# Optimization experiments

Measured on AMD Instinct MI355X. Metric: run time of the kernel, lower is better.

The kernel has to match this reference:

```python
import jax, jax.numpy as jnp
import numpy as np

N_HEAD = 16
T0 = 1.0        # eta schedule reference time
C_LOG = 3.0     # fixed eta(t) = C_LOG * log(t / T0)  (mode='log', non-learnable default)
ETA_CLIP = 50.0 # eta clamped to [-ETA_CLIP, ETA_CLIP] before exponentiation


def setup_inputs() -> dict:
    key = jax.random.key(0)
    k0, k1, k2 = jax.random.split(key, 3)
    B, T, D = 2, 2048, 1024
    x = jax.random.normal(k0, (B, T, D), dtype=jnp.float32)
    ln_weight = jnp.ones((D,), dtype=jnp.float32)  # LayerNorm weight (bias=False per cfg)
    c_attn_w = jax.random.normal(k1, (3 * D, D), dtype=jnp.float32) * 0.02  # torch Linear weight [3D, D]
    c_proj_w = jax.random.normal(k2, (D, D), dtype=jnp.float32) * 0.02      # output proj [D, D]
    # theta_h = inv_softplus(1.0) so that step size h = softplus(theta_h) = 1.0
    theta_h = jnp.asarray(np.log(np.expm1(1.0)), dtype=jnp.float32)
    return {"x": x, "ln_weight": ln_weight, "c_attn_w": c_attn_w,
            "c_proj_w": c_proj_w, "theta_h": theta_h}


def _layer_norm(x, w, eps=1e-5):
    mu = jnp.mean(x, axis=-1, keepdims=True)
    var = jnp.var(x, axis=-1, keepdims=True)
    return (x - mu) * jax.lax.rsqrt(var + eps) * w


def reference(x, ln_weight, c_attn_w, c_proj_w, theta_h):
    B, T, D = x.shape
    H = N_HEAD
    hd = D // H

    y = _layer_norm(x, ln_weight)
    qkv = jnp.einsum('btd,ed->bte', y, c_attn_w)        # [B, T, 3D]
    q, k, v = jnp.split(qkv, 3, axis=-1)
    q = q.reshape(B, T, H, hd).transpose(0, 2, 1, 3)    # [B, H, T, hd]
    k = k.reshape(B, T, H, hd).transpose(0, 2, 1, 3)
    v = v.reshape(B, T, H, hd).transpose(0, 2, 1, 3)

    # time-dependent conformal/symplectic scaling: t_i = t0 + h*i, eta = c_log*log(t/t0)
    h = jax.nn.softplus(theta_h)
    t = T0 + h * jnp.arange(T, dtype=jnp.float32)
    eta = jnp.clip(C_LOG * jnp.log(t / T0), -ETA_CLIP, ETA_CLIP)  # [T]
    q = q * jnp.exp(eta)[None, None, :, None]    # query scaled by exp(+eta(t_i))
    k = k * jnp.exp(-eta)[None, None, :, None]   # key scaled by exp(-eta(t_j))

    att = jnp.einsum('bhqd,bhkd->bhqk', q, k) / jnp.sqrt(jnp.float32(hd))
    mask = jnp.tril(jnp.ones((T, T), dtype=bool))  # causal: keep j <= i
    att = jnp.where(mask[None, None], att, -jnp.inf)
    att = jax.nn.softmax(att, axis=-1)

    out = jnp.einsum('bhqk,bhkd->bhqd', att, v)
    out = out.transpose(0, 2, 1, 3).reshape(B, T, D)
    return jnp.einsum('btd,ed->bte', out, c_proj_w)
```

## Files before the change

kernel.cpp:

```cpp
#include <hip/hip_runtime.h>
#include <stdint.h>
#include <stddef.h>

typedef __attribute__((ext_vector_type(8))) short short8;
typedef __attribute__((ext_vector_type(4))) float float4v;

#define T_SEQ 2048
#define D_MODEL 1024
#define NH 16
#define HD 64

static __device__ __forceinline__ unsigned short f2bf(float f) {
  unsigned u = __builtin_bit_cast(unsigned, f);
  u += 0x7fffu + ((u >> 16) & 1u);
  return (unsigned short)(u >> 16);
}
static __device__ __forceinline__ float bf2f(unsigned short h) {
  unsigned u = ((unsigned)h) << 16;
  return __builtin_bit_cast(float, u);
}
static __device__ __forceinline__ float4v mfma16(short8 a, short8 b, float4v c) {
  return __builtin_amdgcn_mfma_f32_16x16x32_bf16(a, b, c, 0, 0, 0);
}
static __device__ __forceinline__ void split3(float f, unsigned short& h0,
                                              unsigned short& h1, unsigned short& h2) {
  h0 = f2bf(f);
  float r1 = f - bf2f(h0);
  h1 = f2bf(r1);
  float r2 = r1 - bf2f(h1);
  h2 = f2bf(r2);
}
static __device__ __forceinline__ void split2(float f, unsigned short& h0, unsigned short& h1) {
  h0 = f2bf(f);
  h1 = f2bf(f - bf2f(h0));
}

static __device__ __forceinline__ void stage16(const unsigned short* g, unsigned short* l) {
#if __has_builtin(__builtin_amdgcn_global_load_lds)
  __builtin_amdgcn_global_load_lds(
      (const __attribute__((address_space(1))) unsigned int*)g,
      (__attribute__((address_space(3))) unsigned int*)l, 16, 0, 0);
#else
  *(short8*)l = *(const short8*)g;
#endif
}

__global__ __launch_bounds__(256) void prep_kernel(
    const float* x, const float* wgt, const float* attn_w, const float* theta,
    unsigned short* y0, unsigned short* y1, unsigned short* y2,
    unsigned short* W0, unsigned short* W1, unsigned short* W2,
    float* E, float* Einv) {
  __shared__ float rs[4], rq[4];
  int bx = blockIdx.x;
  int tid = threadIdx.x;
  if (bx < 4096) {
    int row = bx;
    const float* xr = x + (size_t)row * D_MODEL;
    float v[4];
    float sum = 0.f, ssq = 0.f;
    for (int it = 0; it < 4; ++it) {
      float f = xr[tid + 256 * it];
      v[it] = f;
      sum += f; ssq += f * f;
    }
    for (int off = 32; off >= 1; off >>= 1) {
      sum += __shfl_xor(sum, off, 64);
      ssq += __shfl_xor(ssq, off, 64);
    }
    int w = tid >> 6;
    if ((tid & 63) == 0) { rs[w] = sum; rq[w] = ssq; }
    __syncthreads();
    sum = rs[0] + rs[1] + rs[2] + rs[3];
    ssq = rq[0] + rq[1] + rq[2] + rq[3];
    float mu = sum * (1.0f / D_MODEL);
    float var = ssq * (1.0f / D_MODEL) - mu * mu;
    float rstd = rsqrtf(var + 1e-5f);
    for (int it = 0; it < 4; ++it) {
      int d = tid + 256 * it;
      float y = (v[it] - mu) * rstd * wgt[d];
      unsigned short h0, h1, h2;
      split3(y, h0, h1, h2);
      size_t o = (size_t)row * D_MODEL + d;
      y0[o] = h0; y1[o] = h1; y2[o] = h2;
    }
  } else if (bx < 5632) {
    size_t base = ((size_t)(bx - 4096) * 256 + tid) * 8;
    int row = (int)(base >> 10);
    short8 a, b, c;
    for (int j = 0; j < 8; ++j) {
      unsigned short h0, h1, h2;
      split3(attn_w[base + j], h0, h1, h2);
      a[j] = (short)h0; b[j] = (short)h1; c[j] = (short)h2;
    }
    *(short8*)(W0 + base) = a;
    *(short8*)(W1 + base) = b;
    if (row < 2048) *(short8*)(W2 + base) = c;
  } else {
    int i = (bx - 5632) * 256 + tid;
    if (i < T_SEQ) {
      float th = theta[0];
      float h = log1pf(expf(th));
      float t = 1.0f + h * (float)i;
      float eta = 3.0f * logf(t);
      eta = fminf(fmaxf(eta, -50.0f), 50.0f);
      E[i] = expf(eta);
      Einv[i] = expf(-eta);
    }
  }
}

__global__ __launch_bounds__(256) void conv_pw(const float* src, unsigned short* P0,
                                               unsigned short* P1) {
  size_t base = ((size_t)blockIdx.x * 256 + threadIdx.x) * 8;
  short8 a, b;
  for (int j = 0; j < 8; ++j) {
    unsigned short h0, h1;
    split2(src[base + j], h0, h1);
    a[j] = (short)h0; b[j] = (short)h1;
  }
  *(short8*)(P0 + base) = a;
  *(short8*)(P1 + base) = b;
}

__global__ __launch_bounds__(256) void qkv_gemm(
    const unsigned short* y0, const unsigned short* y1, const unsigned short* y2,
    const unsigned short* W0, const unsigned short* W1, const unsigned short* W2,
    const float* E, const float* Einv,
    float* Qf, unsigned short* K0, unsigned short* K1, unsigned short* K2,
    unsigned short* VbT) {
  __shared__ unsigned short SB[6 * 4096];
  int tid = threadIdx.x;
  int w = tid >> 6, lane = tid & 63, q4 = lane >> 4, ln = lane & 15;
  int wr = w >> 1, wc = w & 1;
  int m0 = blockIdx.y * 128;
  int bi = m0 >> 11;
  int m0g = m0 & 2047;
  int srow = tid >> 2, kpart = tid & 3;
  unsigned lds_off = (unsigned)tid * 16;
  float4v zero = {0.f, 0.f, 0.f, 0.f};
  float4v acc[4][4];
  for (int mt = 0; mt < 4; ++mt)
    for (int ct = 0; ct < 4; ++ct) acc[mt][ct] = zero;

  if (blockIdx.x < 16) {
    int n0g = blockIdx.x * 128;
    const unsigned short* Asrc[3] = {y0, y1, y2};
    const unsigned short* Bsrc[3] = {W0, W1, W2};
    for (int k0 = 0; k0 < D_MODEL; k0 += 32) {
      __syncthreads();
      for (int i = 0; i < 2; ++i) {
        size_t arow = (size_t)(m0 + srow + i * 64) * D_MODEL + k0 + kpart * 8;
        size_t brow = (size_t)(n0g + srow + i * 64) * D_MODEL + k0 + kpart * 8;
        for (int s = 0; s < 3; ++s) {
          stage16(Asrc[s] + arow, (unsigned short*)((char*)(SB + s * 4096) + lds_off + i * 4096));
          stage16(Bsrc[s] + brow, (unsigned short*)((char*)(SB + (3 + s) * 4096) + lds_off + i * 4096));
        }
      }
      __syncthreads();
      short8 af[4][3];
      for (int mt = 0; mt < 4; ++mt)
        for (int s = 0; s < 3; ++s)
          af[mt][s] = *(const short8*)(SB + s * 4096 + (wr * 64 + mt * 16 + ln) * 32 + q4 * 8);
      for (int ct = 0; ct < 4; ++ct) {
        int brow = (wc * 64 + ct * 16 + ln) * 32 + q4 * 8;
        short8 b0 = *(const short8*)(SB + 3 * 4096 + brow);
        short8 b1 = *(const short8*)(SB + 4 * 4096 + brow);
        short8 b2 = *(const short8*)(SB + 5 * 4096 + brow);
        for (int mt = 0; mt < 4; ++mt) {
          float4v a = acc[mt][ct];
          a = mfma16(af[mt][0], b0, a);
          a = mfma16(af[mt][1], b0, a);
          a = mfma16(af[mt][0], b1, a);
          a = mfma16(af[mt][1], b1, a);
          a = mfma16(af[mt][0], b2, a);
          a = mfma16(af[mt][2], b0, a);
          acc[mt][ct] = a;
        }
      }
    }
    int region = n0g >> 10;
    __syncthreads();
    if (region == 0) {
      float* Ql = (float*)SB;
      for (int h = 0; h < 2; ++h) {
        if (wc == h) {
          for (int mt = 0; mt < 4; ++mt)
            for (int ct = 0; ct < 4; ++ct)
              for (int r = 0; r < 4; ++r) {
                int t_loc = wr * 64 + mt * 16 + q4 * 4 + r;
                int d = ct * 16 + ln;
                int t = m0g + t_loc;
                Ql[t_loc * 64 + d] = acc[mt][ct][r] * (E[t] * 0.1803368801f);
              }
        }
        __syncthreads();
        int h_glob = ((n0g + h * 64) & 1023) >> 6;
        float* dst = Qf + ((size_t)(bi * NH + h_glob) * T_SEQ + m0g) * HD;
        for (int it = 0; it < 8; ++it) {
          int idx = it * 256 + tid;
          *(float4v*)(dst + idx * 4) = *(const float4v*)(Ql + idx * 4);
        }
        __syncthreads();
      }
    } else {
      unsigned short* Kl = SB;
      for (int h = 0; h < 2; ++h) {
        if (wc == h) {
          for (int mt = 0; mt < 4; ++mt)
            for (int ct = 0; ct < 4; ++ct)
              for (int r = 0; r < 4; ++r) {
                int t_loc = wr * 64 + mt * 16 + q4 * 4 + r;
                int d = ct * 16 + ln;
                int t = m0g + t_loc;
                unsigned short h0, h1, h2;
                split3(acc[mt][ct][r] * Einv[t], h0, h1, h2);
                Kl[t_loc * 64 + d] = h0;
                Kl[8192 + t_loc * 64 + d] = h1;
                Kl[16384 + t_loc * 64 + d] = h2;
              }
        }
        __syncthreads();
        int h_glob = ((n0g + h * 64) & 1023) >> 6;
        size_t base = ((size_t)(bi * NH + h_glob) * T_SEQ + m0g) * HD;
        unsigned short* dsts[3] = {K0 + base, K1 + base, K2 + base};
        for (int s = 0; s < 3; ++s)
          for (int it = 0; it < 4; ++it) {
            int idx = it * 256 + tid;
            *(short8*)(dsts[s] + idx * 8) = *(const short8*)(Kl + s * 8192 + idx * 8);
          }
        __syncthreads();
      }
    }
  } else {
    int n0g = (blockIdx.x - 16) * 128;
    const unsigned short* Asrc[2] = {y0, y1};
    const unsigned short* Bsrc[2] = {W0, W1};
    for (int k0 = 0; k0 < D_MODEL; k0 += 32) {
      __syncthreads();
      for (int i = 0; i < 2; ++i) {
        size_t arow = (size_t)(m0 + srow + i * 64) * D_MODEL + k0 + kpart * 8;
        size_t brow = (size_t)(2048 + n0g + srow + i * 64) * D_MODEL + k0 + kpart * 8;
        for (int s = 0; s < 2; ++s) {
          stage16(Asrc[s] + arow, (unsigned short*)((char*)(SB + s * 4096) + lds_off + i * 4096));
          stage16(Bsrc[s] + brow, (unsigned short*)((char*)(SB + (2 + s) * 4096) + lds_off + i * 4096));
        }
      }
      __syncthreads();
      short8 af[4][2];
      for (int mt = 0; mt < 4; ++mt)
        for (int s = 0; s < 2; ++s)
          af[mt][s] = *(const short8*)(SB + s * 4096 + (wr * 64 + mt * 16 + ln) * 32 + q4 * 8);
      for (int ct = 0; ct < 4; ++ct) {
        int brow = (wc * 64 + ct * 16 + ln) * 32 + q4 * 8;
        short8 b0 = *(const short8*)(SB + 2 * 4096 + brow);
        short8 b1 = *(const short8*)(SB + 3 * 4096 + brow);
        for (int mt = 0; mt < 4; ++mt) {
          float4v a = acc[mt][ct];
          a = mfma16(af[mt][0], b0, a);
          a = mfma16(af[mt][1], b0, a);
          a = mfma16(af[mt][0], b1, a);
          acc[mt][ct] = a;
        }
      }
    }
    __syncthreads();
    unsigned short* Vl = SB;
    for (int h = 0; h < 2; ++h) {
      if (wc == h) {
        for (int mt = 0; mt < 4; ++mt)
          for (int ct = 0; ct < 4; ++ct)
            for (int r = 0; r < 4; ++r) {
              int t_loc = wr * 64 + mt * 16 + q4 * 4 + r;
              int d = ct * 16 + ln;
              Vl[d * 128 + t_loc] = f2bf(acc[mt][ct][r]);
            }
      }
      __syncthreads();
      int h_glob = (n0g + h * 64) >> 6;
      size_t base = (size_t)(bi * NH + h_glob) * HD * T_SEQ + m0g;
      for (int it = 0; it < 4; ++it) {
        int idx = it * 256 + tid;
        int d = idx >> 4, c = idx & 15;
        *(short8*)(VbT + base + (size_t)d * T_SEQ + c * 8) =
            *(const short8*)(Vl + d * 128 + c * 8);
      }
      __syncthreads();
    }
  }
}

#define ATTN_STAGE(BUF, J0)                                                   \
  for (int i_ = 0; i_ < 2; ++i_) {                                            \
    size_t go_ = (size_t)((J0) + srow + i_ * 32) * 64 + scd * 8;              \
    int lo_ = tid * 8 + i_ * 2048;                                            \
    stage16(Kb0 + go_, &Ks[BUF][0][lo_]);                                     \
    stage16(Kb1 + go_, &Ks[BUF][1][lo_]);                                     \
    stage16(Kb2 + go_, &Ks[BUF][2][lo_]);                                     \
    stage16(Vb + (size_t)(srow + i_ * 32) * T_SEQ + (J0) + scd * 8,           \
            &Vs[BUF][lo_]);                                                   \
  }

#define ATTN_STEP(JT, DIAG)                                                   \
  {                                                                           \
    const int cur_ = (JT) & 1;                                                \
    float p[4][4];                                                            \
    for (int c = 0; c < 4; ++c) {                                             \
      float4v s = zero;                                                       \
      for (int ks = 0; ks < 2; ++ks) {                                        \
        int koff = ((c * 16 + ln) * 8 + ((ks * 4 + q4) ^ swz)) * 8;           \
        short8 k0v = *(const short8*)&Ks[cur_][0][koff];                      \
        short8 k1v = *(const short8*)&Ks[cur_][1][koff];                      \
        short8 k2v = *(const short8*)&Ks[cur_][2][koff];                      \
        s = mfma16(qa[ks][0], k0v, s);                                        \
        s = mfma16(qa[ks][1], k0v, s);                                        \
        s = mfma16(qa[ks][0], k1v, s);                                        \
        s = mfma16(qa[ks][1], k1v, s);                                        \
        s = mfma16(qa[ks][0], k2v, s);                                        \
        s = mfma16(qa[ks][2], k0v, s);                                        \
      }                                                                       \
      if (DIAG) {                                                             \
        int jrow = (JT) * 64 + c * 16 + ln;                                   \
        for (int r = 0; r < 4; ++r)                                           \
          if (jrow > ibase + q4 * 4 + r) s[r] = -3e38f;                       \
      }                                                                       \
      for (int r = 0; r < 4; ++r) p[c][r] = s[r];                             \
    }                                                                         \
    float alpha[4], mnew[4];                                                  \
    for (int r = 0; r < 4; ++r) {                                             \
      float tm = fmaxf(fmaxf(p[0][r], p[1][r]), fmaxf(p[2][r], p[3][r]));     \
      for (int off = 8; off >= 1; off >>= 1)                                  \
        tm = fmaxf(tm, __shfl_xor(tm, off, 16));                              \
      mnew[r] = fmaxf(m_r[r], tm);                                            \
      alpha[r] = exp2f(m_r[r] - mnew[r]);                                     \
      m_r[r] = mnew[r];                                                       \
    }                                                                         \
    for (int c = 0; c < 4; ++c)                                               \
      for (int r = 0; r < 4; ++r) p[c][r] = exp2f(p[c][r] - mnew[r]);         \
    for (int c = 0; c < 4; ++c)                                               \
      for (int r = 0; r < 4; ++r) oacc[c][r] *= alpha[r];                     \
    for (int r = 0; r < 4; ++r) lacc[r] *= alpha[r];                          \
    __asm__ __volatile__("" ::: "memory");                                    \
    for (int c = 0; c < 4; ++c)                                               \
      for (int r = 0; r < 4; ++r)                                             \
        Plds[w][q4 * 4 + r][c * 16 + ln] =                                    \
            (unsigned short)(__builtin_bit_cast(unsigned, p[c][r]) >> 16);    \
    __asm__ __volatile__("" ::: "memory");                                    \
    for (int ks = 0; ks < 2; ++ks) {                                          \
      short8 pa = *(const short8*)&Plds[w][ln][ks * 32 + q4 * 8];             \
      for (int c = 0; c < 4; ++c) {                                           \
        int voff = ((c * 16 + ln) * 8 + ((ks * 4 + q4) ^ swz)) * 8;           \
        short8 vb = *(const short8*)&Vs[cur_][voff];                          \
        oacc[c] = mfma16(pa, vb, oacc[c]);                                    \
      }                                                                       \
      lacc = mfma16(pa, ones, lacc);                                          \
    }                                                                         \
    __asm__ __volatile__("" ::: "memory");                                    \
  }

__global__ __launch_bounds__(256) void attn_kernel(
    const float* Qf, const unsigned short* K0, const unsigned short* K1,
    const unsigned short* K2, const unsigned short* VbT,
    unsigned short* Ob0, unsigned short* Ob1) {
  __shared__ unsigned short Ks[2][3][4096];
  __shared__ unsigned short Vs[2][4096];
  __shared__ unsigned short Plds[4][16][72];
  int tid = threadIdx.x;
  int w = tid >> 6, lane = tid & 63, q4 = lane >> 4, ln = lane & 15;
  int bidx = blockIdx.x;
  int bh = ((bidx & 7) << 2) | ((bidx >> 3) & 3);
  int px = bidx >> 5;
  const float* Qb = Qf + (size_t)bh * T_SEQ * HD;
  const unsigned short* Kb0 = K0 + (size_t)bh * T_SEQ * HD;
  const unsigned short* Kb1 = K1 + (size_t)bh * T_SEQ * HD;
  const unsigned short* Kb2 = K2 + (size_t)bh * T_SEQ * HD;
  const unsigned short* Vb = VbT + (size_t)bh * HD * T_SEQ;
  int b = bh >> 4, hh = bh & 15;
  float4v zero = {0.f, 0.f, 0.f, 0.f};
  short8 ones;
  for (int j = 0; j < 8; ++j) ones[j] = (short)(unsigned short)0x3F80;

  int srow = tid >> 3, scs = tid & 7;
  int scd = scs ^ (srow & 7);
  int swz = ln & 7;

  for (int half = 0; half < 2; ++half) {
    int qt = half ? (31 - px) : px;
    int q0 = qt * 64;
    int ibase = q0 + w * 16;

    short8 qa[2][3];
    {
      const float* qp = Qb + (size_t)(ibase + ln) * HD;
      for (int ks = 0; ks < 2; ++ks) {
        float f[8];
        *(float4v*)&f[0] = *(const float4v*)(qp + ks * 32 + q4 * 8);
        *(float4v*)&f[4] = *(const float4v*)(qp + ks * 32 + q4 * 8 + 4);
        for (int j = 0; j < 8; ++j) {
          unsigned short h0, h1, h2;
          split3(f[j], h0, h1, h2);
          qa[ks][0][j] = (short)h0; qa[ks][1][j] = (short)h1; qa[ks][2][j] = (short)h2;
        }
      }
    }

    float m_r[4] = {-3e38f, -3e38f, -3e38f, -3e38f};
    float4v lacc = zero;
    float4v oacc[4];
    for (int c = 0; c < 4; ++c) oacc[c] = zero;

    __syncthreads();
    ATTN_STAGE(0, 0)
    for (int jt = 0; jt < qt; ++jt) {
      __syncthreads();
      ATTN_STAGE((jt + 1) & 1, (jt + 1) * 64)
      ATTN_STEP(jt, 0)
    }
    __syncthreads();
    ATTN_STEP(qt, 1)

    for (int c = 0; c < 4; ++c)
      for (int r = 0; r < 4; ++r) {
        int i = ibase + q4 * 4 + r;
        float val = oacc[c][r] / lacc[r];
        unsigned short h0, h1;
        split2(val, h0, h1);
        size_t o = ((size_t)(b * T_SEQ + i)) * D_MODEL + hh * 64 + c * 16 + ln;
        Ob0[o] = h0; Ob1[o] = h1;
      }
  }
}
#undef ATTN_STAGE
#undef ATTN_STEP

__global__ __launch_bounds__(256) void proj_gemm(
    const unsigned short* A0, const unsigned short* A1,
    const unsigned short* P0, const unsigned short* P1, float* out) {
  __shared__ unsigned short SB[4 * 4096];
  int tid = threadIdx.x;
  int w = tid >> 6, lane = tid & 63, q4 = lane >> 4, ln = lane & 15;
  int wr = w >> 1, wc = w & 1;
  int n0g = blockIdx.x * 128;
  int m0 = blockIdx.y * 128;
  const unsigned short* Asrc[2] = {A0, A1};
  const unsigned short* Bsrc[2] = {P0, P1};

  float4v zero = {0.f, 0.f, 0.f, 0.f};
  float4v acc[4][4];
  for (int mt = 0; mt < 4; ++mt)
    for (int ct = 0; ct < 4; ++ct) acc[mt][ct] = zero;

  int srow = tid >> 2, kpart = tid & 3;
  unsigned lds_off = (unsigned)tid * 16;

  for (int k0 = 0; k0 < D_MODEL; k0 += 32) {
    __syncthreads();
    for (int i = 0; i < 2; ++i) {
      size_t arow = (size_t)(m0 + srow + i * 64) * D_MODEL + k0 + kpart * 8;
      size_t brow = (size_t)(n0g + srow + i * 64) * D_MODEL + k0 + kpart * 8;
      for (int s = 0; s < 2; ++s) {
        stage16(Asrc[s] + arow, (unsigned short*)((char*)(SB + s * 4096) + lds_off + i * 4096));
        stage16(Bsrc[s] + brow, (unsigned short*)((char*)(SB + (2 + s) * 4096) + lds_off + i * 4096));
      }
    }
    __syncthreads();

    short8 af[4][2];
    for (int mt = 0; mt < 4; ++mt)
      for (int s = 0; s < 2; ++s)
        af[mt][s] = *(const short8*)(SB + s * 4096 + (wr * 64 + mt * 16 + ln) * 32 + q4 * 8);
    for (int ct = 0; ct < 4; ++ct) {
      int brow = (wc * 64 + ct * 16 + ln) * 32 + q4 * 8;
      short8 b0 = *(const short8*)(SB + 2 * 4096 + brow);
      short8 b1 = *(const short8*)(SB + 3 * 4096 + brow);
      for (int mt = 0; mt < 4; ++mt) {
        float4v a = acc[mt][ct];
        a = mfma16(af[mt][0], b0, a);
        a = mfma16(af[mt][1], b0, a);
        a = mfma16(af[mt][0], b1, a);
        acc[mt][ct] = a;
      }
    }
  }

  for (int mt = 0; mt < 4; ++mt)
    for (int ct = 0; ct < 4; ++ct)
      for (int r = 0; r < 4; ++r) {
        int gm = m0 + wr * 64 + mt * 16 + q4 * 4 + r;
        int col = n0g + wc * 64 + ct * 16 + ln;
        out[(size_t)gm * D_MODEL + col] = acc[mt][ct][r];
      }
}

extern "C" void kernel_launch(void* const* d_in, const int* in_sizes, int n_in,
                              void* d_out, int out_size, void* d_ws, size_t ws_size,
                              hipStream_t stream) {
  const float* x      = (const float*)d_in[0];
  const float* ln_w   = (const float*)d_in[1];
  const float* attn_w = (const float*)d_in[2];
  const float* proj_w = (const float*)d_in[3];
  const float* theta  = (const float*)d_in[4];
  float* out = (float*)d_out;

  char* ws = (char*)d_ws;
  const size_t SZY  = (size_t)4096 * 1024 * 2;
  const size_t SZW  = (size_t)3072 * 1024 * 2;
  const size_t SZW2 = (size_t)2048 * 1024 * 2;
  const size_t SZQ  = (size_t)2 * 16 * 2048 * 64 * 4;
  const size_t SZK  = (size_t)2 * 16 * 2048 * 64 * 2;

  unsigned short* y0 = (unsigned short*)(ws);
  unsigned short* y1 = (unsigned short*)(ws + SZY);
  unsigned short* y2 = (unsigned short*)(ws + 2 * SZY);
  unsigned short* W0 = (unsigned short*)(ws + 3 * SZY);
  unsigned short* W1 = (unsigned short*)(ws + 3 * SZY + SZW);
  unsigned short* W2 = (unsigned short*)(ws + 3 * SZY + 2 * SZW);
  float* Qf          = (float*)(ws + 3 * SZY + 2 * SZW + SZW2);
  unsigned short* K0 = (unsigned short*)(ws + 3 * SZY + 2 * SZW + SZW2 + SZQ);
  unsigned short* K1 = (unsigned short*)(ws + 3 * SZY + 2 * SZW + SZW2 + SZQ + SZK);
  float* E           = (float*)(ws + 3 * SZY + 2 * SZW + SZW2 + SZQ + 2 * SZK);
  float* Einv        = E + T_SEQ;
  unsigned short* Ob0 = y0;
  unsigned short* Ob1 = y1;
  unsigned short* PW0 = y2;
  unsigned short* PW1 = y2 + (size_t)1024 * 1024;
  unsigned short* VbT = (unsigned short*)d_out;
  unsigned short* K2  = (unsigned short*)((char*)d_out + SZK);

  size_t needed = 3 * SZY + 2 * SZW + SZW2 + SZQ + 2 * SZK + 2 * T_SEQ * 4;
  if (ws_size < needed) return;

  prep_kernel<<<dim3(5640), dim3(256), 0, stream>>>(x, ln_w, attn_w, theta,
                                                    y0, y1, y2, W0, W1, W2, E, Einv);
  qkv_gemm<<<dim3(24, 32), dim3(256), 0, stream>>>(y0, y1, y2, W0, W1, W2, E, Einv,
                                                   Qf, K0, K1, K2, VbT);
  conv_pw<<<dim3(512), dim3(256), 0, stream>>>(proj_w, PW0, PW1);
  attn_kernel<<<dim3(512), dim3(256), 0, stream>>>(Qf, K0, K1, K2, VbT, Ob0, Ob1);
  proj_gemm<<<dim3(8, 32), dim3(256), 0, stream>>>(Ob0, Ob1, PW0, PW1, out);
}
```

Baseline: 374.8 us.

## Rewrite QKV GEMM as 256x128-tile double-buffered kernel with swizzled LDS

Replaces the QKV projection GEMM with a 512-thread kernel using 256x128 tiles, K-step 64, and double-buffered LDS. The split-bf16 precision terms are flattened into a linear sequence of K tiles. Global-to-LDS staging of the next tiles is interleaved with MFMA phases through explicit barriers, setprio and vmcnt waits, and LDS columns are XOR-swizzled to avoid bank conflicts. Block IDs are remapped for locality. The goal is to hide load latency and cut sync overhead per MFMA, at the cost of 96KB of dynamic LDS and tight hand scheduling that may limit occupancy.

```diff
diff --git a/kernel.cpp b/kernel.cpp
--- a/kernel.cpp
+++ b/kernel.cpp
@@ -122,172 +122,238 @@
   *(short8*)(P1 + base) = b;
 }
 
-__global__ __launch_bounds__(256) void qkv_gemm(
-    const unsigned short* y0, const unsigned short* y1, const unsigned short* y2,
-    const unsigned short* W0, const unsigned short* W1, const unsigned short* W2,
-    const float* E, const float* Einv,
-    float* Qf, unsigned short* K0, unsigned short* K1, unsigned short* K2,
-    unsigned short* VbT) {
-  __shared__ unsigned short SB[6 * 4096];
+
+template <int MA, int MB, int KS>
+static __device__ __forceinline__ void mfma_row2(float4v (&acc)[4][4],
+                                                 const short8 (&afr)[4][2],
+                                                 const short8 (&bfr)[4][2]) {
+  __builtin_amdgcn_s_setprio(1);
+#pragma unroll
+  for (int nf = 0; nf < 4; ++nf)
+    acc[MA][nf] = mfma16(afr[MA][KS], bfr[nf][KS], acc[MA][nf]);
+#pragma unroll
+  for (int nf = 0; nf < 4; ++nf)
+    acc[MB][nf] = mfma16(afr[MB][KS], bfr[nf][KS], acc[MB][nf]);
+  __builtin_amdgcn_s_setprio(0);
+}
+
+#define RD_A(BF, MF, KS)                                                        \
+  (*(const short8*)(lds_u + (BF) * 24576 + ((wm * 64 + (MF) * 16 + ln) * 64) +  \
+                    ((((KS) * 4 + q4) ^ lnl) * 8)))
+#define RD_B(BF, NF, KS)                                                        \
+  (*(const short8*)(lds_u + (BF) * 24576 + 16384 +                              \
+                    ((wn * 64 + (NF) * 16 + ln) * 64) +                         \
+                    ((((KS) * 4 + q4) ^ lnl) * 8)))
+
+#define STG_A(BF, AP, KI)                                                       \
+  do {                                                                          \
+    const unsigned short* g0 = (AP) + (size_t)(m0 + srow8) * 1024 + (KI) + scol8; \
+    stage16(g0, lds_u + (BF) * 24576 + tid * 8);                                \
+    stage16(g0 + 64 * 1024, lds_u + (BF) * 24576 + 4096 + tid * 8);             \
+    stage16(g0 + 128 * 1024, lds_u + (BF) * 24576 + 8192 + tid * 8);            \
+    stage16(g0 + 192 * 1024, lds_u + (BF) * 24576 + 12288 + tid * 8);           \
+  } while (0)
+
+#define STG_B(BF, BP, KI)                                                       \
+  do {                                                                          \
+    const unsigned short* g0 = (BP) + (size_t)(brow0 + srow8) * 1024 + (KI) + scol8; \
+    stage16(g0, lds_u + (BF) * 24576 + 16384 + tid * 8);                        \
+    stage16(g0 + 64 * 1024, lds_u + (BF) * 24576 + 16384 + 4096 + tid * 8);     \
+  } while (0)
+
+#define ASEL(tb) ((tb) == 5 ? y2 : (((tb) & 1) ? y1 : y0))
+#define BSEL(tb) (isV ? ((tb) < 2 ? W0 : W1)                                    \
+                      : ((tb) < 2 ? W0 : ((tb) < 4 ? W1 : ((tb) == 4 ? W2 : W0))))
+
+#define SBAR __builtin_amdgcn_s_barrier()
+#define SCHED0 __builtin_amdgcn_sched_barrier(0)
+
+#define PHASES4(BF, A2P, B2P, KI2)                                              \
+                       \
+  afr[0][0] = RD_A(BF, 0, 0); afr[1][0] = RD_A(BF, 1, 0);                       \
+  bfr[0][0] = RD_B(BF, 0, 0); bfr[1][0] = RD_B(BF, 1, 0);                       \
+  bfr[2][0] = RD_B(BF, 2, 0); bfr[3][0] = RD_B(BF, 3, 0);                       \
+  SCHED0; SBAR;                                                                 \
+  mfma_row2<0, 1, 0>(acc, afr, bfr);                                            \
+  SCHED0; SBAR;                                                                 \
+                       \
+  afr[2][0] = RD_A(BF, 2, 0); afr[3][0] = RD_A(BF, 3, 0);                       \
+  afr[0][1] = RD_A(BF, 0, 1); afr[1][1] = RD_A(BF, 1, 1);                       \
+  afr[2][1] = RD_A(BF, 2, 1); afr[3][1] = RD_A(BF, 3, 1);                       \
+  SCHED0; SBAR;                                                                 \
+  mfma_row2<2, 3, 0>(acc, afr, bfr);                                            \
+  SCHED0; SBAR;                                                                 \
+          \
+  bfr[0][1] = RD_B(BF, 0, 1); bfr[1][1] = RD_B(BF, 1, 1);                       \
+  bfr[2][1] = RD_B(BF, 2, 1); bfr[3][1] = RD_B(BF, 3, 1);                       \
+  if (pref) { STG_A(BF, A2P, KI2); }                                            \
+  SCHED0; SBAR;                                                                 \
+  mfma_row2<0, 1, 1>(acc, afr, bfr);                                            \
+  SCHED0; SBAR;                                                                 \
+             \
+  if (pref) { STG_B(BF, B2P, KI2); }                                            \
+  SCHED0; SBAR;                                                                 \
+  mfma_row2<2, 3, 1>(acc, afr, bfr);                                            \
+  SCHED0;                                                                       \
+  if (pref) { asm volatile("s_waitcnt vmcnt(6)" ::: "memory"); }                \
+  else      { asm volatile("s_waitcnt vmcnt(0)" ::: "memory"); }                \
+  SBAR;
+
+__global__ __launch_bounds__(512, 2) void qkv8(
+    const unsigned short* __restrict__ y0, const unsigned short* __restrict__ y1,
+    const unsigned short* __restrict__ y2, const unsigned short* __restrict__ W0,
+    const unsigned short* __restrict__ W1, const unsigned short* __restrict__ W2,
+    const float* __restrict__ E, const float* __restrict__ Einv,
+    float* __restrict__ Qf, unsigned short* __restrict__ K0,
+    unsigned short* __restrict__ K1, unsigned short* __restrict__ K2,
+    unsigned short* __restrict__ VbT) {
+  extern __shared__ unsigned short lds_u[];
   int tid = threadIdx.x;
   int w = tid >> 6, lane = tid & 63, q4 = lane >> 4, ln = lane & 15;
-  int wr = w >> 1, wc = w & 1;
-  int m0 = blockIdx.y * 128;
-  int bi = m0 >> 11;
-  int m0g = m0 & 2047;
-  int srow = tid >> 2, kpart = tid & 3;
-  unsigned lds_off = (unsigned)tid * 16;
+  int lnl = ln & 7;
+  int wm = w >> 1, wn = w & 1;
+
+  int bid = blockIdx.x, bx, by;
+  if (bid < 256) {
+    int wg = ((bid & 7) << 5) | (bid >> 3);
+    by = wg >> 4; bx = wg & 15;
+  } else {
+    int vid = bid - 256;
+    int wg = ((vid & 7) << 4) | (vid >> 3);
+    by = wg >> 3; bx = 16 + (wg & 7);
+  }
+  int m0 = by * 256;
+  bool isV = (bx >= 16);
+  int NKT = isV ? 48 : 96;
+  int brow0 = isV ? (2048 + (bx - 16) * 128) : bx * 128;
+
+  int srow8 = tid >> 3;
+  int scol8 = ((tid & 7) ^ (srow8 & 7)) * 8;
+
   float4v zero = {0.f, 0.f, 0.f, 0.f};
   float4v acc[4][4];
-  for (int mt = 0; mt < 4; ++mt)
-    for (int ct = 0; ct < 4; ++ct) acc[mt][ct] = zero;
-
-  if (blockIdx.x < 16) {
-    int n0g = blockIdx.x * 128;
-    const unsigned short* Asrc[3] = {y0, y1, y2};
-    const unsigned short* Bsrc[3] = {W0, W1, W2};
-    for (int k0 = 0; k0 < D_MODEL; k0 += 32) {
+#pragma unroll
+  for (int mf = 0; mf < 4; ++mf)
+#pragma unroll
+    for (int nf = 0; nf < 4; ++nf) acc[mf][nf] = zero;
+  short8 afr[4][2], bfr[4][2];
+
+  {
+    const unsigned short* Ap = ASEL(0);
+    const unsigned short* Bp = BSEL(0);
+    STG_A(0, Ap, 0);
+    STG_B(0, Bp, 0);
+    STG_A(1, Ap, 64);
+    STG_B(1, Bp, 64);
+  }
+  asm volatile("s_waitcnt vmcnt(6)" ::: "memory");
+  SBAR;
+
+  int NIT = NKT >> 1;
+  for (int it = 0; it < NIT; ++it) {
+    const int a2 = 2 * it + 2;
+    const bool pref = (a2 < NKT);
+    const unsigned short *Aa2 = y0, *Ba2 = W0, *Ab2 = y0, *Bb2 = W0;
+    int kia2 = 0, kib2 = 0;
+    if (pref) {
+      int ta = a2 >> 4, tb = (a2 + 1) >> 4;
+      Aa2 = ASEL(ta); Ba2 = BSEL(ta); kia2 = (a2 & 15) << 6;
+      Ab2 = ASEL(tb); Bb2 = BSEL(tb); kib2 = ((a2 + 1) & 15) << 6;
+    }
+    PHASES4(0, Aa2, Ba2, kia2)
+    PHASES4(1, Ab2, Bb2, kib2)
+  }
+
+  int bi = m0 >> 11, m0g = m0 & 2047;
+  if (bx < 8) {
+    float* Ql = (float*)lds_u;
+    for (int g = 0; g < 2; ++g) {
+      if (wn == g) {
+#pragma unroll
+        for (int mf = 0; mf < 4; ++mf)
+#pragma unroll
+          for (int nf = 0; nf < 4; ++nf)
+#pragma unroll
+            for (int r = 0; r < 4; ++r) {
+              int rl = wm * 64 + mf * 16 + q4 * 4 + r;
+              int t = m0g + rl;
+              Ql[rl * 64 + nf * 16 + ln] = acc[mf][nf][r] * (E[t] * 0.1803368801f);
+            }
+      }
       __syncthreads();
-      for (int i = 0; i < 2; ++i) {
-        size_t arow = (size_t)(m0 + srow + i * 64) * D_MODEL + k0 + kpart * 8;
-        size_t brow = (size_t)(n0g + srow + i * 64) * D_MODEL + k0 + kpart * 8;
-        for (int s = 0; s < 3; ++s) {
-          stage16(Asrc[s] + arow, (unsigned short*)((char*)(SB + s * 4096) + lds_off + i * 4096));
-          stage16(Bsrc[s] + brow, (unsigned short*)((char*)(SB + (3 + s) * 4096) + lds_off + i * 4096));
-        }
+      int h = bx * 2 + g;
+      float* dst = Qf + ((size_t)(bi * NH + h) * T_SEQ + m0g) * HD;
+      for (int itc = 0; itc < 8; ++itc) {
+        int idx = itc * 512 + tid;
+        *(float4v*)(dst + idx * 4) = *(const float4v*)(Ql + idx * 4);
       }
       __syncthreads();
-      short8 af[4][3];
-      for (int mt = 0; mt < 4; ++mt)
-        for (int s = 0; s < 3; ++s)
-          af[mt][s] = *(const short8*)(SB + s * 4096 + (wr * 64 + mt * 16 + ln) * 32 + q4 * 8);
-      for (int ct = 0; ct < 4; ++ct) {
-        int brow = (wc * 64 + ct * 16 + ln) * 32 + q4 * 8;
-        short8 b0 = *(const short8*)(SB + 3 * 4096 + brow);
-        short8 b1 = *(const short8*)(SB + 4 * 4096 + brow);
-        short8 b2 = *(const short8*)(SB + 5 * 4096 + brow);
-        for (int mt = 0; mt < 4; ++mt) {
-          float4v a = acc[mt][ct];
-          a = mfma16(af[mt][0], b0, a);
-          a = mfma16(af[mt][1], b0, a);
-          a = mfma16(af[mt][0], b1, a);
-          a = mfma16(af[mt][1], b1, a);
-          a = mfma16(af[mt][0], b2, a);
-          a = mfma16(af[mt][2], b0, a);
-          acc[mt][ct] = a;
-        }
-      }
-    }
-    int region = n0g >> 10;
-    __syncthreads();
-    if (region == 0) {
-      float* Ql = (float*)SB;
-      for (int h = 0; h < 2; ++h) {
-        if (wc == h) {
-          for (int mt = 0; mt < 4; ++mt)
-            for (int ct = 0; ct < 4; ++ct)
-              for (int r = 0; r < 4; ++r) {
-                int t_loc = wr * 64 + mt * 16 + q4 * 4 + r;
-                int d = ct * 16 + ln;
-                int t = m0g + t_loc;
-                Ql[t_loc * 64 + d] = acc[mt][ct][r] * (E[t] * 0.1803368801f);
-              }
-        }
-        __syncthreads();
-        int h_glob = ((n0g + h * 64) & 1023) >> 6;
-        float* dst = Qf + ((size_t)(bi * NH + h_glob) * T_SEQ + m0g) * HD;
-        for (int it = 0; it < 8; ++it) {
-          int idx = it * 256 + tid;
-          *(float4v*)(dst + idx * 4) = *(const float4v*)(Ql + idx * 4);
-        }
-        __syncthreads();
-      }
-    } else {
-      unsigned short* Kl = SB;
-      for (int h = 0; h < 2; ++h) {
-        if (wc == h) {
-          for (int mt = 0; mt < 4; ++mt)
-            for (int ct = 0; ct < 4; ++ct)
-              for (int r = 0; r < 4; ++r) {
-                int t_loc = wr * 64 + mt * 16 + q4 * 4 + r;
-                int d = ct * 16 + ln;
-                int t = m0g + t_loc;
-                unsigned short h0, h1, h2;
-                split3(acc[mt][ct][r] * Einv[t], h0, h1, h2);
-                Kl[t_loc * 64 + d] = h0;
-                Kl[8192 + t_loc * 64 + d] = h1;
-                Kl[16384 + t_loc * 64 + d] = h2;
-              }
-        }
-        __syncthreads();
-        int h_glob = ((n0g + h * 64) & 1023) >> 6;
-        size_t base = ((size_t)(bi * NH + h_glob) * T_SEQ + m0g) * HD;
-        unsigned short* dsts[3] = {K0 + base, K1 + base, K2 + base};
-        for (int s = 0; s < 3; ++s)
-          for (int it = 0; it < 4; ++it) {
-            int idx = it * 256 + tid;
-            *(short8*)(dsts[s] + idx * 8) = *(const short8*)(Kl + s * 8192 + idx * 8);
-          }
-        __syncthreads();
-      }
+    }
+  } else if (bx < 16) {
+    unsigned short* Kl = lds_u;
+    for (int g = 0; g < 2; ++g) {
+      if (wn == g) {
+#pragma unroll
+        for (int mf = 0; mf < 4; ++mf)
+#pragma unroll
+          for (int nf = 0; nf < 4; ++nf)
+#pragma unroll
+            for (int r = 0; r < 4; ++r) {
+              int rl = wm * 64 + mf * 16 + q4 * 4 + r;
+              int t = m0g + rl;
+              unsigned short h0, h1, h2;
+              split3(acc[mf][nf][r] * Einv[t], h0, h1, h2);
+              int o = rl * 64 + nf * 16 + ln;
+              Kl[o] = h0; Kl[16384 + o] = h1; Kl[32768 + o] = h2;
+            }
+      }
+      __syncthreads();
+      int h = (bx - 8) * 2 + g;
+      size_t base = ((size_t)(bi * NH + h) * T_SEQ + m0g) * HD;
+      for (int itc = 0; itc < 4; ++itc) {
+        int idx = itc * 512 + tid;
+        *(short8*)(K0 + base + idx * 8) = *(const short8*)(Kl + idx * 8);
+        *(short8*)(K1 + base + idx * 8) = *(const short8*)(Kl + 16384 + idx * 8);
+        *(short8*)(K2 + base + idx * 8) = *(const short8*)(Kl + 32768 + idx * 8);
+      }
+      __syncthreads();
     }
   } else {
-    int n0g = (blockIdx.x - 16) * 128;
-    const unsigned short* Asrc[2] = {y0, y1};
-    const unsigned short* Bsrc[2] = {W0, W1};
-    for (int k0 = 0; k0 < D_MODEL; k0 += 32) {
+    unsigned short* Vl = lds_u;
+    for (int g = 0; g < 2; ++g) {
+      if (wn == g) {
+#pragma unroll
+        for (int mf = 0; mf < 4; ++mf)
+#pragma unroll
+          for (int nf = 0; nf < 4; ++nf)
+#pragma unroll
+            for (int r = 0; r < 4; ++r) {
+              int rl = wm * 64 + mf * 16 + q4 * 4 + r;
+              int d = nf * 16 + ln;
+              Vl[d * 256 + rl] = f2bf(acc[mf][nf][r]);
+            }
+      }
       __syncthreads();
-      for (int i = 0; i < 2; ++i) {
-        size_t arow = (size_t)(m0 + srow + i * 64) * D_MODEL + k0 + kpart * 8;
-        size_t brow = (size_t)(2048 + n0g + srow + i * 64) * D_MODEL + k0 + kpart * 8;
-        for (int s = 0; s < 2; ++s) {
-          stage16(Asrc[s] + arow, (unsigned short*)((char*)(SB + s * 4096) + lds_off + i * 4096));
-          stage16(Bsrc[s] + brow, (unsigned short*)((char*)(SB + (2 + s) * 4096) + lds_off + i * 4096));
-        }
+      int h = (bx - 16) * 2 + g;
+      unsigned short* dst = VbT + (size_t)(bi * NH + h) * HD * T_SEQ + m0g;
+      for (int itc = 0; itc < 4; ++itc) {
+        int idx = itc * 512 + tid;
+        int d = idx >> 5, c = idx & 31;
+        *(short8*)(dst + (size_t)d * T_SEQ + c * 8) = *(const short8*)(Vl + d * 256 + c * 8);
       }
       __syncthreads();
-      short8 af[4][2];
-      for (int mt = 0; mt < 4; ++mt)
-        for (int s = 0; s < 2; ++s)
-          af[mt][s] = *(const short8*)(SB + s * 4096 + (wr * 64 + mt * 16 + ln) * 32 + q4 * 8);
-      for (int ct = 0; ct < 4; ++ct) {
-        int brow = (wc * 64 + ct * 16 + ln) * 32 + q4 * 8;
-        short8 b0 = *(const short8*)(SB + 2 * 4096 + brow);
-        short8 b1 = *(const short8*)(SB + 3 * 4096 + brow);
-        for (int mt = 0; mt < 4; ++mt) {
-          float4v a = acc[mt][ct];
-          a = mfma16(af[mt][0], b0, a);
-          a = mfma16(af[mt][1], b0, a);
-          a = mfma16(af[mt][0], b1, a);
-          acc[mt][ct] = a;
-        }
-      }
-    }
-    __syncthreads();
-    unsigned short* Vl = SB;
-    for (int h = 0; h < 2; ++h) {
-      if (wc == h) {
-        for (int mt = 0; mt < 4; ++mt)
-          for (int ct = 0; ct < 4; ++ct)
-            for (int r = 0; r < 4; ++r) {
-              int t_loc = wr * 64 + mt * 16 + q4 * 4 + r;
-              int d = ct * 16 + ln;
-              Vl[d * 128 + t_loc] = f2bf(acc[mt][ct][r]);
-            }
-      }
-      __syncthreads();
-      int h_glob = (n0g + h * 64) >> 6;
-      size_t base = (size_t)(bi * NH + h_glob) * HD * T_SEQ + m0g;
-      for (int it = 0; it < 4; ++it) {
-        int idx = it * 256 + tid;
-        int d = idx >> 4, c = idx & 15;
-        *(short8*)(VbT + base + (size_t)d * T_SEQ + c * 8) =
-            *(const short8*)(Vl + d * 128 + c * 8);
-      }
-      __syncthreads();
-    }
-  }
-}
+    }
+  }
+}
+#undef RD_A
+#undef RD_B
+#undef STG_A
+#undef STG_B
+#undef ASEL
+#undef BSEL
+#undef PHASES4
+#undef SBAR
+#undef SCHED0
 
 #define ATTN_STAGE(BUF, J0)                                                   \
   for (int i_ = 0; i_ < 2; ++i_) {                                            \
@@ -529,10 +595,17 @@
   size_t needed = 3 * SZY + 2 * SZW + SZW2 + SZQ + 2 * SZK + 2 * T_SEQ * 4;
   if (ws_size < needed) return;
 
+  static int lds_cfg = 0;
+  if (!lds_cfg) {
+    hipFuncSetAttribute((const void*)qkv8,
+                        hipFuncAttributeMaxDynamicSharedMemorySize, 98304);
+    lds_cfg = 1;
+  }
+
   prep_kernel<<<dim3(5640), dim3(256), 0, stream>>>(x, ln_w, attn_w, theta,
                                                     y0, y1, y2, W0, W1, W2, E, Einv);
-  qkv_gemm<<<dim3(24, 32), dim3(256), 0, stream>>>(y0, y1, y2, W0, W1, W2, E, Einv,
-                                                   Qf, K0, K1, K2, VbT);
+  qkv8<<<dim3(384), dim3(512), 98304, stream>>>(y0, y1, y2, W0, W1, W2, E, Einv,
+                                                Qf, K0, K1, K2, VbT);
   conv_pw<<<dim3(512), dim3(256), 0, stream>>>(proj_w, PW0, PW1);
   attn_kernel<<<dim3(512), dim3(256), 0, stream>>>(Qf, K0, K1, K2, VbT, Ob0, Ob1);
   proj_gemm<<<dim3(8, 32), dim3(256), 0, stream>>>(Ob0, Ob1, PW0, PW1, out);
```

Result: slower. 384.8 us (+2.7%).
